# Kernel optimization log

Hardware: AMD Instinct MI355X
Metric: run time of the kernel (lower is better)

Reference implementation:

```python
import jax, jax.numpy as jnp
import numpy as np

DIM = 512
HID = 4 * DIM
E = 8
B, T = 2, 2048


def setup_inputs() -> dict:
    key = jax.random.key(0)
    ks = jax.random.split(key, 8)
    s = 0.02
    x = jax.random.normal(ks[0], (B, T, DIM), dtype=jnp.float32)
    route = jax.random.randint(ks[1], (B * T,), 0, E, dtype=jnp.int32)
    # stacked per-expert params; Linear y = x @ W + b with W in [in, out] layout
    w_in = jax.random.normal(ks[2], (E, DIM, HID), dtype=jnp.float32) * s
    b_in = jnp.zeros((E, HID), dtype=jnp.float32)
    w_gate = jax.random.normal(ks[3], (E, DIM, HID), dtype=jnp.float32) * s
    b_gate = jnp.zeros((E, HID), dtype=jnp.float32)
    w_out = jax.random.normal(ks[4], (E, HID, DIM), dtype=jnp.float32) * s
    b_out = jnp.zeros((E, DIM), dtype=jnp.float32)
    return {"x": x, "route": route, "w_in": w_in, "b_in": b_in,
            "w_gate": w_gate, "b_gate": b_gate, "w_out": w_out, "b_out": b_out}


def reference(x, route, w_in, b_in, w_gate, b_gate, w_out, b_out):
    Bb, Tt, C = x.shape
    xf = x.reshape(-1, C)  # [N, C]
    out = jnp.zeros_like(xf)
    n_experts = w_in.shape[0]
    # loop over the small fixed expert set; each expert is a SwiGLU FFN,
    # output scattered back by masking (same math as output[idx] += expert(x[idx]))
    for e in range(n_experts):
        mask = (route == e).astype(xf.dtype)[:, None]  # [N, 1]
        h = jax.nn.silu(xf @ w_gate[e] + b_gate[e]) * (xf @ w_in[e] + b_in[e])  # [N, 4C]
        out = out + mask * (h @ w_out[e] + b_out[e])
    return out.reshape(Bb, Tt, C)
```

## Files before the change

kernel.cpp:

```cpp
#include <hip/hip_runtime.h>

#define DIM 512
#define HID 2048
#define NEXP 8

typedef __attribute__((ext_vector_type(8))) short v8s;
typedef __attribute__((ext_vector_type(4))) float v4f;

__device__ __forceinline__ unsigned short f2bf(float f) {
  union { __bf16 b; unsigned short u; } c;
  c.b = (__bf16)f;
  return c.u;
}

__device__ __forceinline__ void gload16(const void* g, void* l) {
  __builtin_amdgcn_global_load_lds(
      (const __attribute__((address_space(1))) unsigned int*)g,
      (__attribute__((address_space(3))) unsigned int*)l, 16, 0, 0);
}

__global__ void route_prep(const int* __restrict__ route, int* __restrict__ meta, int ntok) {
  __shared__ int c[NEXP];
  int t = threadIdx.x;
  if (t < NEXP) c[t] = 0;
  __syncthreads();
  for (int n = t; n < ntok; n += blockDim.x) atomicAdd(&c[route[n]], 1);
  __syncthreads();
  if (t == 0) {
    int acc = 0, pacc = 0;
    for (int e = 0; e < NEXP; ++e) {
      meta[e] = c[e];
      meta[NEXP + e] = acc;
      meta[2 * NEXP + e] = acc;
      meta[3 * NEXP + e] = pacc;
      acc += c[e];
      pacc += ((c[e] + 127) >> 7) << 7;
    }
  }
}

__global__ void fill_perm(const int* __restrict__ route, int* __restrict__ meta,
                          int* __restrict__ perm, int ntok) {
  int n = blockIdx.x * blockDim.x + threadIdx.x;
  if (n < ntok) {
    int p = atomicAdd(&meta[2 * NEXP + route[n]], 1);
    perm[p] = n;
  }
}

__global__ __launch_bounds__(256) void x_conv(
    const float* __restrict__ x, const int* __restrict__ meta,
    const int* __restrict__ perm, unsigned short* __restrict__ xp)
{
  const int bid = blockIdx.x;
  const int e = bid & 7;
  const int mt = bid >> 3;
  const int cnt = meta[e];
  if (mt * 64 >= cnt) return;
  const int off  = meta[NEXP + e];
  const int poff = meta[3 * NEXP + e];
  const int t = threadIdx.x;
  const int r = t & 63, q = t >> 6;
  int arow = mt * 64 + r; if (arow >= cnt) arow = cnt - 1;
  const float* src = x + (size_t)perm[off + arow] * DIM + q * 128;
  unsigned short* dst = xp + (size_t)((poff + mt * 64) >> 6) * 32768;
  #pragma unroll
  for (int j = 0; j < 16; ++j) {
    float4 f0 = ((const float4*)src)[2 * j];
    float4 f1 = ((const float4*)src)[2 * j + 1];
    v8s v;
    v[0] = (short)f2bf(f0.x); v[1] = (short)f2bf(f0.y);
    v[2] = (short)f2bf(f0.z); v[3] = (short)f2bf(f0.w);
    v[4] = (short)f2bf(f1.x); v[5] = (short)f2bf(f1.y);
    v[6] = (short)f2bf(f1.z); v[7] = (short)f2bf(f1.w);
    *(v8s*)(dst + (size_t)((q * 16 + j) * 64 + r) * 8) = v;
  }
}

__global__ __launch_bounds__(256, 3) void gemm1p(
    const unsigned short* __restrict__ xp,
    const float* __restrict__ wg_, const float* __restrict__ bg_,
    const float* __restrict__ wi_, const float* __restrict__ bi_,
    const int* __restrict__ meta,
    unsigned short* __restrict__ hbuf)
{
  const int bid = blockIdx.x;
  const int e = bid & 7;
  const int r_ = bid >> 3;
  const int j = r_ & 15;
  const int mt = r_ >> 4;
  const int cnt = meta[e];
  const int m0 = mt * 64;
  if (m0 >= cnt) return;
  const int poff = meta[3 * NEXP + e];
  const int n0 = j * 128;

  __shared__ __align__(16) unsigned char lds[40960];

  const int t = threadIdx.x;
  const int l = t & 63, w = t >> 6;
  const int wm = w >> 1, wn = w & 1;
  const int fr = l & 15, fg = l >> 4;

  const unsigned short* pa = xp + (size_t)((poff + m0) >> 6) * 32768;
  const float* wg = wg_ + (size_t)e * DIM * HID + n0;
  const float* wi = wi_ + (size_t)e * DIM * HID + n0;

  const int s_kq = t >> 7;
  const int s_n  = t & 127;

  v4f aG[2][4], aI[2][4];
  #pragma unroll
  for (int i = 0; i < 2; ++i)
    #pragma unroll
    for (int q = 0; q < 4; ++q) {
      aG[i][q] = (v4f){0.f, 0.f, 0.f, 0.f};
      aI[i][q] = (v4f){0.f, 0.f, 0.f, 0.f};
    }

  float stG0[8], stG1[8], stI0[8], stI1[8];

  auto wload = [&](int s) {
    const size_t b0 = (size_t)(s * 32 + s_kq * 8) * HID + s_n;
    const size_t b1 = (size_t)(s * 32 + (s_kq + 2) * 8) * HID + s_n;
    #pragma unroll
    for (int q = 0; q < 8; ++q) {
      stG0[q] = wg[b0 + (size_t)q * HID];
      stG1[q] = wg[b1 + (size_t)q * HID];
      stI0[q] = wi[b0 + (size_t)q * HID];
      stI1[q] = wi[b1 + (size_t)q * HID];
    }
  };
  auto wstore = [&](int b) {
    unsigned char* base = lds + b * 20480;
    v8s g0, g1, i0, i1;
    #pragma unroll
    for (int q = 0; q < 8; ++q) {
      g0[q] = (short)f2bf(stG0[q]); g1[q] = (short)f2bf(stG1[q]);
      i0[q] = (short)f2bf(stI0[q]); i1[q] = (short)f2bf(stI1[q]);
    }
    *(v8s*)(base + 4096  + (s_kq * 128 + s_n) * 16)       = g0;
    *(v8s*)(base + 4096  + ((s_kq + 2) * 128 + s_n) * 16) = g1;
    *(v8s*)(base + 12288 + (s_kq * 128 + s_n) * 16)       = i0;
    *(v8s*)(base + 12288 + ((s_kq + 2) * 128 + s_n) * 16) = i1;
  };
  auto aload = [&](int s, int b) {
    gload16(pa + ((size_t)(s * 4 + w) * 64 + l) * 8, lds + b * 20480 + t * 16);
  };

  wload(0);
  wstore(0);
  aload(0, 0);
  __builtin_amdgcn_sched_barrier(0);
  wload(1);
  asm volatile("s_waitcnt vmcnt(32) lgkmcnt(0)" ::: "memory");
  __builtin_amdgcn_sched_barrier(0);
  __builtin_amdgcn_s_barrier();
  __builtin_amdgcn_sched_barrier(0);

  int cur = 0;
  for (int s = 0; s < 16; ++s) {
    const unsigned char* base = lds + cur * 20480;
    v8s af[2], gf[4], inf[4];
    #pragma unroll
    for (int mf = 0; mf < 2; ++mf)
      af[mf] = *(const v8s*)(base + (fg * 64 + wm * 32 + mf * 16 + fr) * 16);
    #pragma unroll
    for (int nf = 0; nf < 4; ++nf) {
      gf[nf]  = *(const v8s*)(base + 4096  + (fg * 128 + wn * 64 + nf * 16 + fr) * 16);
      inf[nf] = *(const v8s*)(base + 12288 + (fg * 128 + wn * 64 + nf * 16 + fr) * 16);
    }
    #pragma unroll
    for (int mf = 0; mf < 2; ++mf)
      #pragma unroll
      for (int nf = 0; nf < 4; ++nf) {
        aG[mf][nf] = __builtin_amdgcn_mfma_f32_16x16x32_bf16(af[mf], gf[nf],  aG[mf][nf], 0, 0, 0);
        aI[mf][nf] = __builtin_amdgcn_mfma_f32_16x16x32_bf16(af[mf], inf[nf], aI[mf][nf], 0, 0, 0);
      }
    if (s < 15) {
      aload(s + 1, cur ^ 1);
      __builtin_amdgcn_sched_barrier(0);
      wstore(cur ^ 1);
      if (s < 14) {
        wload(s + 2);
        asm volatile("s_waitcnt vmcnt(32) lgkmcnt(0)" ::: "memory");
      } else {
        asm volatile("s_waitcnt vmcnt(0) lgkmcnt(0)" ::: "memory");
      }
      __builtin_amdgcn_sched_barrier(0);
      __builtin_amdgcn_s_barrier();
      __builtin_amdgcn_sched_barrier(0);
    }
    cur ^= 1;
  }

  const size_t tb = (size_t)((poff + m0) >> 6) * 131072;
  #pragma unroll
  for (int nf = 0; nf < 4; ++nf) {
    const int c = n0 + wn * 64 + nf * 16 + fr;
    const float bg = bg_[(size_t)e * HID + c];
    const float bi = bi_[(size_t)e * HID + c];
    #pragma unroll
    for (int mf = 0; mf < 2; ++mf)
      #pragma unroll
      for (int jj = 0; jj < 4; ++jj) {
        const int r = wm * 32 + mf * 16 + fg * 4 + jj;
        const float g = aG[mf][nf][jj] + bg;
        const float v = aI[mf][nf][jj] + bi;
        const float hval = g / (1.f + __expf(-g)) * v;
        hbuf[tb + (size_t)((c >> 3) * 64 + r) * 8 + (c & 7)] = f2bf(hval);
      }
  }
}

__global__ __launch_bounds__(256, 4) void gemm2p(
    const unsigned short* __restrict__ hbuf,
    const float* __restrict__ wo_, const float* __restrict__ bo_,
    const int* __restrict__ meta, const int* __restrict__ perm,
    float* __restrict__ out)
{
  const int bid = blockIdx.x;
  const int e = bid & 7;
  const int r_ = bid >> 3;
  const int jn = r_ & 15;
  const int mt = r_ >> 4;
  const int cnt = meta[e];
  const int m0 = mt * 64;
  if (m0 >= cnt) return;
  const int off = meta[NEXP + e], poff = meta[3 * NEXP + e];
  const int n0 = jn * 32;

  __shared__ __align__(16) unsigned char lds[24576];

  const int t = threadIdx.x;
  const int l = t & 63, w = t >> 6;
  const int wm = w >> 1, wn = w & 1;
  const int fr = l & 15, fg = l >> 4;

  const unsigned short* pa = hbuf + (size_t)((poff + m0) >> 6) * 131072;
  const float* wo = wo_ + (size_t)e * HID * DIM + n0;

  const int b_kq = t >> 5, b_n = t & 31;

  v4f acc[2];
  acc[0] = (v4f){0.f, 0.f, 0.f, 0.f};
  acc[1] = (v4f){0.f, 0.f, 0.f, 0.f};

  float stB[8];
  auto bload = [&](int s) {
    const size_t b0 = (size_t)(s * 64 + b_kq * 8) * DIM + b_n;
    #pragma unroll
    for (int q = 0; q < 8; ++q) stB[q] = wo[b0 + (size_t)q * DIM];
  };
  auto bstore = [&](int b) {
    v8s r;
    #pragma unroll
    for (int q = 0; q < 8; ++q) r[q] = (short)f2bf(stB[q]);
    *(v8s*)(lds + b * 12288 + 8192 + (b_kq * 32 + b_n) * 16) = r;
  };
  auto aload = [&](int s, int b) {
    #pragma unroll
    for (int i = 0; i < 2; ++i)
      gload16(pa + (size_t)s * 4096 + ((size_t)(i * 4 + w) * 64 + l) * 8,
              lds + b * 12288 + ((i * 4 + w) * 64) * 16 + l * 16);
  };

  bload(0);
  bstore(0);
  aload(0, 0);
  __builtin_amdgcn_sched_barrier(0);
  bload(1);
  asm volatile("s_waitcnt vmcnt(8) lgkmcnt(0)" ::: "memory");
  __builtin_amdgcn_sched_barrier(0);
  __builtin_amdgcn_s_barrier();
  __builtin_amdgcn_sched_barrier(0);

  int cur = 0;
  for (int s = 0; s < 32; ++s) {
    const unsigned char* base = lds + cur * 12288;
    v8s af[2][2], bf[2];
    #pragma unroll
    for (int kk = 0; kk < 2; ++kk) {
      #pragma unroll
      for (int mf = 0; mf < 2; ++mf)
        af[kk][mf] = *(const v8s*)(base + ((kk * 4 + fg) * 64 + wm * 32 + mf * 16 + fr) * 16);
      bf[kk] = *(const v8s*)(base + 8192 + ((kk * 4 + fg) * 32 + wn * 16 + fr) * 16);
    }
    #pragma unroll
    for (int kk = 0; kk < 2; ++kk)
      #pragma unroll
      for (int mf = 0; mf < 2; ++mf)
        acc[mf] = __builtin_amdgcn_mfma_f32_16x16x32_bf16(af[kk][mf], bf[kk], acc[mf], 0, 0, 0);
    if (s < 31) {
      aload(s + 1, cur ^ 1);
      __builtin_amdgcn_sched_barrier(0);
      bstore(cur ^ 1);
      if (s < 30) {
        bload(s + 2);
        asm volatile("s_waitcnt vmcnt(8) lgkmcnt(0)" ::: "memory");
      } else {
        asm volatile("s_waitcnt vmcnt(0) lgkmcnt(0)" ::: "memory");
      }
      __builtin_amdgcn_sched_barrier(0);
      __builtin_amdgcn_s_barrier();
      __builtin_amdgcn_sched_barrier(0);
    }
    cur ^= 1;
  }

  const int c = n0 + wn * 16 + fr;
  const float bo = bo_[(size_t)e * DIM + c];
  #pragma unroll
  for (int mf = 0; mf < 2; ++mf)
    #pragma unroll
    for (int jj = 0; jj < 4; ++jj) {
      const int r = wm * 32 + mf * 16 + fg * 4 + jj;
      if (m0 + r < cnt)
        out[(size_t)perm[off + m0 + r] * DIM + c] = acc[mf][jj] + bo;
    }
}

extern "C" void kernel_launch(void* const* d_in, const int* in_sizes, int n_in,
                              void* d_out, int out_size, void* d_ws, size_t ws_size,
                              hipStream_t stream) {
  const float* x      = (const float*)d_in[0];
  const int*   route  = (const int*)d_in[1];
  const float* w_in   = (const float*)d_in[2];
  const float* b_in   = (const float*)d_in[3];
  const float* w_gate = (const float*)d_in[4];
  const float* b_gate = (const float*)d_in[5];
  const float* w_out  = (const float*)d_in[6];
  const float* b_out  = (const float*)d_in[7];
  float* out = (float*)d_out;

  const int ntok = in_sizes[1];

  int* meta = (int*)d_ws;
  int* perm = (int*)((char*)d_ws + 128);

  unsigned short* xp   = (unsigned short*)((char*)d_ws + 65536);
  unsigned short* hbuf = (unsigned short*)((char*)d_ws + 65536 + 5242880);

  const int MT64 = (ntok + 63) / 64;

  route_prep<<<1, 256, 0, stream>>>(route, meta, ntok);
  fill_perm<<<(ntok + 255) / 256, 256, 0, stream>>>(route, meta, perm, ntok);
  x_conv<<<NEXP * MT64, 256, 0, stream>>>(x, meta, perm, xp);
  gemm1p<<<NEXP * 16 * MT64, 256, 0, stream>>>(
      xp, w_gate, b_gate, w_in, b_in, meta, hbuf);
  gemm2p<<<NEXP * 16 * MT64, 256, 0, stream>>>(
      hbuf, w_out, b_out, meta, perm, out);
}
```

Before: 116.4 us.

## Retile expert GEMMs to 128-row M tiles with vectorized fp32 weight staging

Both expert GEMMs now process 128-token M tiles instead of 64. This halves how many times each expert's fp32 weights are re-read and converted per token tile. Weight loads switch from strided scalar loads to float4 row loads, written into LDS as ushort4 pieces. The grid is reordered so expert/N stripes are innermost, and the next A-tile load is issued before the MFMA work. The cost is fewer blocks, more accumulator registers, larger LDS in gemm2, and x_conv padding each expert up to 128 rows, which assumes the per-expert offsets allow 128-row tiles.

```diff
diff --git a/kernel.cpp b/kernel.cpp
--- a/kernel.cpp
+++ b/kernel.cpp
@@ -56,7 +56,8 @@
   const int e = bid & 7;
   const int mt = bid >> 3;
   const int cnt = meta[e];
-  if (mt * 64 >= cnt) return;
+  const int padded = ((cnt + 127) >> 7) << 7;
+  if (mt * 64 >= padded) return;
   const int off  = meta[NEXP + e];
   const int poff = meta[3 * NEXP + e];
   const int t = threadIdx.x;
@@ -77,7 +78,7 @@
   }
 }
 
-__global__ __launch_bounds__(256, 3) void gemm1p(
+__global__ __launch_bounds__(256, 3) void gemm1n(
     const unsigned short* __restrict__ xp,
     const float* __restrict__ wg_, const float* __restrict__ bg_,
     const float* __restrict__ wi_, const float* __restrict__ bi_,
@@ -85,67 +86,69 @@
     unsigned short* __restrict__ hbuf)
 {
   const int bid = blockIdx.x;
-  const int e = bid & 7;
-  const int r_ = bid >> 3;
-  const int j = r_ & 15;
-  const int mt = r_ >> 4;
+  const int stripe = bid & 255;
+  const int mt = bid >> 8;
+  const int e = stripe >> 5, j = stripe & 31;
   const int cnt = meta[e];
-  const int m0 = mt * 64;
+  const int m0 = mt * 128;
   if (m0 >= cnt) return;
   const int poff = meta[3 * NEXP + e];
-  const int n0 = j * 128;
-
-  __shared__ __align__(16) unsigned char lds[40960];
+  const int n0 = j * 64;
+
+  __shared__ __align__(16) unsigned char lds[32768];
 
   const int t = threadIdx.x;
   const int l = t & 63, w = t >> 6;
   const int wm = w >> 1, wn = w & 1;
   const int fr = l & 15, fg = l >> 4;
 
-  const unsigned short* pa = xp + (size_t)((poff + m0) >> 6) * 32768;
-  const float* wg = wg_ + (size_t)e * DIM * HID + n0;
-  const float* wi = wi_ + (size_t)e * DIM * HID + n0;
-
-  const int s_kq = t >> 7;
-  const int s_n  = t & 127;
-
-  v4f aG[2][4], aI[2][4];
-  #pragma unroll
-  for (int i = 0; i < 2; ++i)
-    #pragma unroll
-    for (int q = 0; q < 4; ++q) {
+  const int tile0 = (poff + m0) >> 6;
+
+  const int ko = t & 7, nq = t >> 3;
+  const int wcol = (nq & 15) * 4;
+  const float* wsrc = ((nq < 16) ? wg_ : wi_) + (size_t)e * DIM * HID + n0 + wcol;
+  const int wpan = 8192 + ((nq < 16) ? 0 : 4096);
+  const int woct = ko >> 1, whalf = ko & 1;
+
+  v4f aG[4][2], aI[4][2];
+  #pragma unroll
+  for (int i = 0; i < 4; ++i)
+    #pragma unroll
+    for (int q = 0; q < 2; ++q) {
       aG[i][q] = (v4f){0.f, 0.f, 0.f, 0.f};
       aI[i][q] = (v4f){0.f, 0.f, 0.f, 0.f};
     }
 
-  float stG0[8], stG1[8], stI0[8], stI1[8];
-
+  float4 ld0, ld1, ld2, ld3;
   auto wload = [&](int s) {
-    const size_t b0 = (size_t)(s * 32 + s_kq * 8) * HID + s_n;
-    const size_t b1 = (size_t)(s * 32 + (s_kq + 2) * 8) * HID + s_n;
-    #pragma unroll
-    for (int q = 0; q < 8; ++q) {
-      stG0[q] = wg[b0 + (size_t)q * HID];
-      stG1[q] = wg[b1 + (size_t)q * HID];
-      stI0[q] = wi[b0 + (size_t)q * HID];
-      stI1[q] = wi[b1 + (size_t)q * HID];
-    }
+    const float* b = wsrc + (size_t)(s * 32 + ko * 4) * HID;
+    ld0 = *(const float4*)(b);
+    ld1 = *(const float4*)(b + HID);
+    ld2 = *(const float4*)(b + 2 * HID);
+    ld3 = *(const float4*)(b + 3 * HID);
   };
   auto wstore = [&](int b) {
-    unsigned char* base = lds + b * 20480;
-    v8s g0, g1, i0, i1;
-    #pragma unroll
-    for (int q = 0; q < 8; ++q) {
-      g0[q] = (short)f2bf(stG0[q]); g1[q] = (short)f2bf(stG1[q]);
-      i0[q] = (short)f2bf(stI0[q]); i1[q] = (short)f2bf(stI1[q]);
-    }
-    *(v8s*)(base + 4096  + (s_kq * 128 + s_n) * 16)       = g0;
-    *(v8s*)(base + 4096  + ((s_kq + 2) * 128 + s_n) * 16) = g1;
-    *(v8s*)(base + 12288 + (s_kq * 128 + s_n) * 16)       = i0;
-    *(v8s*)(base + 12288 + ((s_kq + 2) * 128 + s_n) * 16) = i1;
+    unsigned char* base = lds + b * 16384 + wpan;
+    const float* f0 = (const float*)&ld0;
+    const float* f1 = (const float*)&ld1;
+    const float* f2 = (const float*)&ld2;
+    const float* f3 = (const float*)&ld3;
+    #pragma unroll
+    for (int i = 0; i < 4; ++i) {
+      ushort4 v;
+      v.x = f2bf(f0[i]); v.y = f2bf(f1[i]);
+      v.z = f2bf(f2[i]); v.w = f2bf(f3[i]);
+      *(ushort4*)(base + (woct * 64 + wcol + i) * 16 + whalf * 8) = v;
+    }
   };
   auto aload = [&](int s, int b) {
-    gload16(pa + ((size_t)(s * 4 + w) * 64 + l) * 8, lds + b * 20480 + t * 16);
+    #pragma unroll
+    for (int i = 0; i < 2; ++i) {
+      const int c = t + 256 * i;
+      const int kq = c >> 7, m = c & 127;
+      gload16(xp + (size_t)(tile0 + (m >> 6)) * 32768 + ((size_t)(s * 4 + kq) * 64 + (m & 63)) * 8,
+              lds + b * 16384 + c * 16);
+    }
   };
 
   wload(0);
@@ -153,37 +156,37 @@
   aload(0, 0);
   __builtin_amdgcn_sched_barrier(0);
   wload(1);
-  asm volatile("s_waitcnt vmcnt(32) lgkmcnt(0)" ::: "memory");
+  asm volatile("s_waitcnt vmcnt(4) lgkmcnt(0)" ::: "memory");
   __builtin_amdgcn_sched_barrier(0);
   __builtin_amdgcn_s_barrier();
   __builtin_amdgcn_sched_barrier(0);
 
   int cur = 0;
   for (int s = 0; s < 16; ++s) {
-    const unsigned char* base = lds + cur * 20480;
-    v8s af[2], gf[4], inf[4];
-    #pragma unroll
-    for (int mf = 0; mf < 2; ++mf)
-      af[mf] = *(const v8s*)(base + (fg * 64 + wm * 32 + mf * 16 + fr) * 16);
-    #pragma unroll
-    for (int nf = 0; nf < 4; ++nf) {
-      gf[nf]  = *(const v8s*)(base + 4096  + (fg * 128 + wn * 64 + nf * 16 + fr) * 16);
-      inf[nf] = *(const v8s*)(base + 12288 + (fg * 128 + wn * 64 + nf * 16 + fr) * 16);
-    }
-    #pragma unroll
-    for (int mf = 0; mf < 2; ++mf)
-      #pragma unroll
-      for (int nf = 0; nf < 4; ++nf) {
+    if (s < 15) aload(s + 1, cur ^ 1);
+    const unsigned char* base = lds + cur * 16384;
+    v8s af[4], gf[2], inf[2];
+    #pragma unroll
+    for (int mf = 0; mf < 4; ++mf)
+      af[mf] = *(const v8s*)(base + (fg * 128 + wm * 64 + mf * 16 + fr) * 16);
+    #pragma unroll
+    for (int nf = 0; nf < 2; ++nf) {
+      gf[nf]  = *(const v8s*)(base + 8192  + (fg * 64 + wn * 32 + nf * 16 + fr) * 16);
+      inf[nf] = *(const v8s*)(base + 12288 + (fg * 64 + wn * 32 + nf * 16 + fr) * 16);
+    }
+    #pragma unroll
+    for (int mf = 0; mf < 4; ++mf)
+      #pragma unroll
+      for (int nf = 0; nf < 2; ++nf) {
         aG[mf][nf] = __builtin_amdgcn_mfma_f32_16x16x32_bf16(af[mf], gf[nf],  aG[mf][nf], 0, 0, 0);
         aI[mf][nf] = __builtin_amdgcn_mfma_f32_16x16x32_bf16(af[mf], inf[nf], aI[mf][nf], 0, 0, 0);
       }
     if (s < 15) {
-      aload(s + 1, cur ^ 1);
       __builtin_amdgcn_sched_barrier(0);
       wstore(cur ^ 1);
       if (s < 14) {
         wload(s + 2);
-        asm volatile("s_waitcnt vmcnt(32) lgkmcnt(0)" ::: "memory");
+        asm volatile("s_waitcnt vmcnt(4) lgkmcnt(0)" ::: "memory");
       } else {
         asm volatile("s_waitcnt vmcnt(0) lgkmcnt(0)" ::: "memory");
       }
@@ -194,75 +197,92 @@
     cur ^= 1;
   }
 
-  const size_t tb = (size_t)((poff + m0) >> 6) * 131072;
-  #pragma unroll
-  for (int nf = 0; nf < 4; ++nf) {
-    const int c = n0 + wn * 64 + nf * 16 + fr;
+  #pragma unroll
+  for (int nf = 0; nf < 2; ++nf) {
+    const int c = n0 + wn * 32 + nf * 16 + fr;
     const float bg = bg_[(size_t)e * HID + c];
     const float bi = bi_[(size_t)e * HID + c];
     #pragma unroll
-    for (int mf = 0; mf < 2; ++mf)
+    for (int mf = 0; mf < 4; ++mf)
       #pragma unroll
       for (int jj = 0; jj < 4; ++jj) {
-        const int r = wm * 32 + mf * 16 + fg * 4 + jj;
+        const int r = wm * 64 + mf * 16 + fg * 4 + jj;
         const float g = aG[mf][nf][jj] + bg;
         const float v = aI[mf][nf][jj] + bi;
         const float hval = g / (1.f + __expf(-g)) * v;
-        hbuf[tb + (size_t)((c >> 3) * 64 + r) * 8 + (c & 7)] = f2bf(hval);
-      }
-  }
-}
-
-__global__ __launch_bounds__(256, 4) void gemm2p(
+        const int grow = poff + m0 + r;
+        hbuf[(size_t)(grow >> 6) * 131072 + ((size_t)(c >> 3) * 64 + (grow & 63)) * 8 + (c & 7)] = f2bf(hval);
+      }
+  }
+}
+
+__global__ __launch_bounds__(256, 3) void gemm2n(
     const unsigned short* __restrict__ hbuf,
     const float* __restrict__ wo_, const float* __restrict__ bo_,
     const int* __restrict__ meta, const int* __restrict__ perm,
     float* __restrict__ out)
 {
   const int bid = blockIdx.x;
-  const int e = bid & 7;
-  const int r_ = bid >> 3;
-  const int jn = r_ & 15;
-  const int mt = r_ >> 4;
+  const int stripe = bid & 63;
+  const int mt = bid >> 6;
+  const int e = stripe >> 3, jn = stripe & 7;
   const int cnt = meta[e];
-  const int m0 = mt * 64;
+  const int m0 = mt * 128;
   if (m0 >= cnt) return;
   const int off = meta[NEXP + e], poff = meta[3 * NEXP + e];
-  const int n0 = jn * 32;
-
-  __shared__ __align__(16) unsigned char lds[24576];
+  const int n0 = jn * 64;
+
+  __shared__ __align__(16) unsigned char lds[49152];
 
   const int t = threadIdx.x;
   const int l = t & 63, w = t >> 6;
   const int wm = w >> 1, wn = w & 1;
   const int fr = l & 15, fg = l >> 4;
 
-  const unsigned short* pa = hbuf + (size_t)((poff + m0) >> 6) * 131072;
+  const int tile0 = (poff + m0) >> 6;
   const float* wo = wo_ + (size_t)e * HID * DIM + n0;
 
-  const int b_kq = t >> 5, b_n = t & 31;
-
-  v4f acc[2];
-  acc[0] = (v4f){0.f, 0.f, 0.f, 0.f};
-  acc[1] = (v4f){0.f, 0.f, 0.f, 0.f};
-
-  float stB[8];
+  const int ko = t & 15, nq = t >> 4;
+  const int bcol = nq * 4;
+  const int boct = ko >> 1, bhalf = ko & 1;
+
+  v4f acc[4][2];
+  #pragma unroll
+  for (int i = 0; i < 4; ++i) {
+    acc[i][0] = (v4f){0.f, 0.f, 0.f, 0.f};
+    acc[i][1] = (v4f){0.f, 0.f, 0.f, 0.f};
+  }
+
+  float4 ld0, ld1, ld2, ld3;
   auto bload = [&](int s) {
-    const size_t b0 = (size_t)(s * 64 + b_kq * 8) * DIM + b_n;
-    #pragma unroll
-    for (int q = 0; q < 8; ++q) stB[q] = wo[b0 + (size_t)q * DIM];
+    const float* b = wo + (size_t)(s * 64 + ko * 4) * DIM + bcol;
+    ld0 = *(const float4*)(b);
+    ld1 = *(const float4*)(b + DIM);
+    ld2 = *(const float4*)(b + 2 * DIM);
+    ld3 = *(const float4*)(b + 3 * DIM);
   };
   auto bstore = [&](int b) {
-    v8s r;
-    #pragma unroll
-    for (int q = 0; q < 8; ++q) r[q] = (short)f2bf(stB[q]);
-    *(v8s*)(lds + b * 12288 + 8192 + (b_kq * 32 + b_n) * 16) = r;
+    unsigned char* base = lds + b * 24576 + 16384;
+    const float* f0 = (const float*)&ld0;
+    const float* f1 = (const float*)&ld1;
+    const float* f2 = (const float*)&ld2;
+    const float* f3 = (const float*)&ld3;
+    #pragma unroll
+    for (int i = 0; i < 4; ++i) {
+      ushort4 v;
+      v.x = f2bf(f0[i]); v.y = f2bf(f1[i]);
+      v.z = f2bf(f2[i]); v.w = f2bf(f3[i]);
+      *(ushort4*)(base + (boct * 64 + bcol + i) * 16 + bhalf * 8) = v;
+    }
   };
   auto aload = [&](int s, int b) {
     #pragma unroll
-    for (int i = 0; i < 2; ++i)
-      gload16(pa + (size_t)s * 4096 + ((size_t)(i * 4 + w) * 64 + l) * 8,
-              lds + b * 12288 + ((i * 4 + w) * 64) * 16 + l * 16);
+    for (int i = 0; i < 4; ++i) {
+      const int c = t + 256 * i;
+      const int kq = c >> 7, m = c & 127;
+      gload16(hbuf + (size_t)(tile0 + (m >> 6)) * 131072 + ((size_t)(s * 8 + kq) * 64 + (m & 63)) * 8,
+              lds + b * 24576 + c * 16);
+    }
   };
 
   bload(0);
@@ -270,34 +290,36 @@
   aload(0, 0);
   __builtin_amdgcn_sched_barrier(0);
   bload(1);
-  asm volatile("s_waitcnt vmcnt(8) lgkmcnt(0)" ::: "memory");
+  asm volatile("s_waitcnt vmcnt(4) lgkmcnt(0)" ::: "memory");
   __builtin_amdgcn_sched_barrier(0);
   __builtin_amdgcn_s_barrier();
   __builtin_amdgcn_sched_barrier(0);
 
   int cur = 0;
   for (int s = 0; s < 32; ++s) {
-    const unsigned char* base = lds + cur * 12288;
-    v8s af[2][2], bf[2];
+    if (s < 31) aload(s + 1, cur ^ 1);
+    const unsigned char* base = lds + cur * 24576;
     #pragma unroll
     for (int kk = 0; kk < 2; ++kk) {
-      #pragma unroll
-      for (int mf = 0; mf < 2; ++mf)
-        af[kk][mf] = *(const v8s*)(base + ((kk * 4 + fg) * 64 + wm * 32 + mf * 16 + fr) * 16);
-      bf[kk] = *(const v8s*)(base + 8192 + ((kk * 4 + fg) * 32 + wn * 16 + fr) * 16);
-    }
-    #pragma unroll
-    for (int kk = 0; kk < 2; ++kk)
-      #pragma unroll
-      for (int mf = 0; mf < 2; ++mf)
-        acc[mf] = __builtin_amdgcn_mfma_f32_16x16x32_bf16(af[kk][mf], bf[kk], acc[mf], 0, 0, 0);
+      v8s af[4], bf[2];
+      #pragma unroll
+      for (int mf = 0; mf < 4; ++mf)
+        af[mf] = *(const v8s*)(base + ((kk * 4 + fg) * 128 + wm * 64 + mf * 16 + fr) * 16);
+      #pragma unroll
+      for (int nf = 0; nf < 2; ++nf)
+        bf[nf] = *(const v8s*)(base + 16384 + ((kk * 4 + fg) * 64 + wn * 32 + nf * 16 + fr) * 16);
+      #pragma unroll
+      for (int mf = 0; mf < 4; ++mf)
+        #pragma unroll
+        for (int nf = 0; nf < 2; ++nf)
+          acc[mf][nf] = __builtin_amdgcn_mfma_f32_16x16x32_bf16(af[mf], bf[nf], acc[mf][nf], 0, 0, 0);
+    }
     if (s < 31) {
-      aload(s + 1, cur ^ 1);
       __builtin_amdgcn_sched_barrier(0);
       bstore(cur ^ 1);
       if (s < 30) {
         bload(s + 2);
-        asm volatile("s_waitcnt vmcnt(8) lgkmcnt(0)" ::: "memory");
+        asm volatile("s_waitcnt vmcnt(4) lgkmcnt(0)" ::: "memory");
       } else {
         asm volatile("s_waitcnt vmcnt(0) lgkmcnt(0)" ::: "memory");
       }
@@ -308,16 +330,19 @@
     cur ^= 1;
   }
 
-  const int c = n0 + wn * 16 + fr;
-  const float bo = bo_[(size_t)e * DIM + c];
-  #pragma unroll
-  for (int mf = 0; mf < 2; ++mf)
-    #pragma unroll
-    for (int jj = 0; jj < 4; ++jj) {
-      const int r = wm * 32 + mf * 16 + fg * 4 + jj;
-      if (m0 + r < cnt)
-        out[(size_t)perm[off + m0 + r] * DIM + c] = acc[mf][jj] + bo;
-    }
+  #pragma unroll
+  for (int nf = 0; nf < 2; ++nf) {
+    const int c = n0 + wn * 32 + nf * 16 + fr;
+    const float bo = bo_[(size_t)e * DIM + c];
+    #pragma unroll
+    for (int mf = 0; mf < 4; ++mf)
+      #pragma unroll
+      for (int jj = 0; jj < 4; ++jj) {
+        const int r = wm * 64 + mf * 16 + fg * 4 + jj;
+        if (m0 + r < cnt)
+          out[(size_t)perm[off + m0 + r] * DIM + c] = acc[mf][nf][jj] + bo;
+      }
+  }
 }
 
 extern "C" void kernel_launch(void* const* d_in, const int* in_sizes, int n_in,
@@ -341,13 +366,14 @@
   unsigned short* xp   = (unsigned short*)((char*)d_ws + 65536);
   unsigned short* hbuf = (unsigned short*)((char*)d_ws + 65536 + 5242880);
 
-  const int MT64 = (ntok + 63) / 64;
+  const int MT64  = (ntok + 63) / 64;
+  const int MT128 = (ntok + 127) / 128;
 
   route_prep<<<1, 256, 0, stream>>>(route, meta, ntok);
   fill_perm<<<(ntok + 255) / 256, 256, 0, stream>>>(route, meta, perm, ntok);
   x_conv<<<NEXP * MT64, 256, 0, stream>>>(x, meta, perm, xp);
-  gemm1p<<<NEXP * 16 * MT64, 256, 0, stream>>>(
+  gemm1n<<<256 * MT128, 256, 0, stream>>>(
       xp, w_gate, b_gate, w_in, b_in, meta, hbuf);
-  gemm2p<<<NEXP * 16 * MT64, 256, 0, stream>>>(
+  gemm2n<<<64 * MT128, 256, 0, stream>>>(
       hbuf, w_out, b_out, meta, perm, out);
 }
```

New measurement: 140.7 us. +20.9%, slower.
